# Optimization experiments

Measured on AMD Instinct MI355X. Metric: run time of the kernel, lower is better.

## Reference

```python
import jax, jax.numpy as jnp
import numpy as np

B, C, L = 4, 256, 4096
C8 = C // 8

def setup_inputs() -> dict:
    key = jax.random.key(0)
    ks = jax.random.split(key, 8)
    s = 1.0 / np.sqrt(C)
    x = jax.random.normal(ks[0], (B, C, L), dtype=jnp.float32)
    Wq = jax.random.normal(ks[1], (C8, C), dtype=jnp.float32) * s
    bq = jax.random.normal(ks[2], (C8,), dtype=jnp.float32) * s
    Wk = jax.random.normal(ks[3], (C8, C), dtype=jnp.float32) * s
    bk = jax.random.normal(ks[4], (C8,), dtype=jnp.float32) * s
    Wv = jax.random.normal(ks[5], (C, C), dtype=jnp.float32) * s
    bv = jax.random.normal(ks[6], (C,), dtype=jnp.float32) * s
    gamma = jax.random.normal(ks[7], (1,), dtype=jnp.float32) * 0.1
    return {"x": x, "Wq": Wq, "bq": bq, "Wk": Wk, "bk": bk, "Wv": Wv, "bv": bv, "gamma": gamma}

def reference(x, Wq, bq, Wk, bk, Wv, bv, gamma):
    # pointwise conv1d == channel matmul: [O,C] x [B,C,L] -> [B,O,L]
    q = jnp.einsum('oc,bcl->bol', Wq, x) + bq[None, :, None]   # [B, C8, L]
    k = jnp.einsum('oc,bcl->bol', Wk, x) + bk[None, :, None]   # [B, C8, L]
    v = jnp.einsum('oc,bcl->bol', Wv, x) + bv[None, :, None]   # [B, C,  L]
    # attention[b,i,j] = sum_c q[b,c,i] * k[b,c,j]
    attn = jnp.einsum('bci,bcj->bij', q, k)                    # [B, L, L]
    attn = jax.nn.softmax(attn, axis=-1)
    # out[b,c,i] = sum_j v[b,c,j] * attn[b,i,j]
    out = jnp.einsum('bcj,bij->bci', v, attn)                  # [B, C, L]
    return gamma * out + x
```

## Files before the change

### kernel.cpp

```cpp
#include <hip/hip_runtime.h>
#include <math.h>

#define BB 4
#define CC 256
#define LL 4096
#define DD 32
#define LOG2E 1.44269504088896f

typedef __attribute__((ext_vector_type(8))) short short8;
typedef __attribute__((ext_vector_type(4))) short short4v;
typedef __attribute__((ext_vector_type(4))) float f32x4;
typedef __attribute__((ext_vector_type(16))) float f32x16;
typedef __attribute__((ext_vector_type(4))) unsigned int uint4v;
typedef __attribute__((ext_vector_type(2))) unsigned int uint2v;

#define BARRIER() asm volatile("s_waitcnt lgkmcnt(0)\n\ts_barrier" ::: "memory")

__device__ inline float fast_exp2(float x) {
#if __has_builtin(__builtin_amdgcn_exp2f)
  return __builtin_amdgcn_exp2f(x);
#else
  return exp2f(x);
#endif
}

#define PACK8_STORE(EX0,EX1,EX2,EX3,EX4,EX5,EX6,EX7, DSTPTR)                         \
  {                                                                                  \
    unsigned pw0, pw1, pw2, pw3;                                                     \
    asm("v_cvt_pk_bf16_f32 %0, %1, %2" : "=v"(pw0) : "v"(EX0), "v"(EX1));            \
    asm("v_cvt_pk_bf16_f32 %0, %1, %2" : "=v"(pw1) : "v"(EX2), "v"(EX3));            \
    asm("v_cvt_pk_bf16_f32 %0, %1, %2" : "=v"(pw2) : "v"(EX4), "v"(EX5));            \
    asm("v_cvt_pk_bf16_f32 %0, %1, %2" : "=v"(pw3) : "v"(EX6), "v"(EX7));            \
    asm("v_permlane32_swap_b32 %0, %1" : "+v"(pw0), "+v"(pw2));                      \
    asm("v_permlane32_swap_b32 %0, %1" : "+v"(pw1), "+v"(pw3));                      \
    uint4v pu; pu.x = pw0; pu.y = pw1; pu.z = pw2; pu.w = pw3;                       \
    *(uint4v*)(DSTPTR) = pu;                                                         \
  }

__global__ __launch_bounds__(256) void wprep_kernel(
    const float* __restrict__ Wq, const float* __restrict__ Wk, const float* __restrict__ Wv,
    unsigned short* __restrict__ wf)
{
  const int t = threadIdx.x;
  const int g = blockIdx.x * 4 + (t >> 6);
  const int lane = t & 63, ql = lane & 31, hi = lane >> 5;
  const int tile = g >> 4, chunk = g & 15;
  const int cin = chunk * 16 + hi * 8;
  const float* src;
  float sc = 1.0f;
  if (tile == 0)      { src = Wq + (size_t)ql * CC; sc = LOG2E; }
  else if (tile == 1) { src = Wk + (size_t)ql * CC; }
  else                { src = Wv + (size_t)(32 * (tile - 2) + ql) * CC; }
  const f32x4 a = *(const f32x4*)(src + cin);
  const f32x4 b2 = *(const f32x4*)(src + cin + 4);
  unsigned w0, w1, w2, w3;
  const float f0 = a[0] * sc, f1 = a[1] * sc, f2 = a[2] * sc, f3 = a[3] * sc;
  const float f4 = b2[0] * sc, f5 = b2[1] * sc, f6 = b2[2] * sc, f7 = b2[3] * sc;
  asm("v_cvt_pk_bf16_f32 %0, %1, %2" : "=v"(w0) : "v"(f0), "v"(f1));
  asm("v_cvt_pk_bf16_f32 %0, %1, %2" : "=v"(w1) : "v"(f2), "v"(f3));
  asm("v_cvt_pk_bf16_f32 %0, %1, %2" : "=v"(w2) : "v"(f4), "v"(f5));
  asm("v_cvt_pk_bf16_f32 %0, %1, %2" : "=v"(w3) : "v"(f6), "v"(f7));
  uint4v u; u.x = w0; u.y = w1; u.z = w2; u.w = w3;
  *(uint4v*)(wf + ((size_t)g * 64 + lane) * 8) = u;
}

__global__ __launch_bounds__(512, 4) void qkv_kernel(
    const float* __restrict__ x, const unsigned short* __restrict__ wf,
    const float* __restrict__ bq, const float* __restrict__ bk, const float* __restrict__ bv,
    unsigned short* __restrict__ qF, unsigned short* __restrict__ kF,
    unsigned short* __restrict__ vF)
{
  __shared__ __align__(16) unsigned short xb[16 * 64 * 8];

  const int t = threadIdx.x;
  const int w = t >> 6, lane = t & 63, ql = lane & 31, hi = lane >> 5;
  const int blk = blockIdx.x;
  const int b  = (blk & 7) >> 1;
  const int it = ((blk >> 3) << 1) + (blk & 1);
  const int i0 = it * 32;

  #pragma unroll
  for (int e = 0; e < 2; ++e) {
    const int cc = 2 * w + e;
    const float* xs = x + ((size_t)(b * CC + cc * 16 + hi * 8)) * LL + i0 + ql;
    float f[8];
    #pragma unroll
    for (int j = 0; j < 8; ++j) f[j] = xs[(size_t)j * LL];
    unsigned w0, w1, w2, w3;
    asm("v_cvt_pk_bf16_f32 %0, %1, %2" : "=v"(w0) : "v"(f[0]), "v"(f[1]));
    asm("v_cvt_pk_bf16_f32 %0, %1, %2" : "=v"(w1) : "v"(f[2]), "v"(f[3]));
    asm("v_cvt_pk_bf16_f32 %0, %1, %2" : "=v"(w2) : "v"(f[4]), "v"(f[5]));
    asm("v_cvt_pk_bf16_f32 %0, %1, %2" : "=v"(w3) : "v"(f[6]), "v"(f[7]));
    uint4v u; u.x = w0; u.y = w1; u.z = w2; u.w = w3;
    *(uint4v*)&xb[(cc * 64 + lane) * 8] = u;
  }
  __syncthreads();

  const f32x16 z16 = {0.f,0.f,0.f,0.f,0.f,0.f,0.f,0.f,0.f,0.f,0.f,0.f,0.f,0.f,0.f,0.f};

  {
    f32x16 D = z16;
    #pragma unroll
    for (int c = 0; c < 16; ++c) {
      const short8 xc = *(const short8*)&xb[(c * 64 + lane) * 8];
      const short8 wv = *(const short8*)(wf + ((size_t)((2 + w) * 16 + c) * 64 + lane) * 8);
      D = __builtin_amdgcn_mfma_f32_32x32x16_bf16(xc, wv, D, 0, 0, 0);
    }
    const float bvv = bv[32 * w + ql];
    #pragma unroll
    for (int r = 0; r < 16; ++r) D[r] += bvv;
    #pragma unroll
    for (int s = 0; s < 2; ++s) {
      unsigned short* dst = vF + (((size_t)(b * 256 + 2 * it + s) * 8 + w) * 64 + lane) * 8;
      PACK8_STORE(D[8*s+0], D[8*s+1], D[8*s+2], D[8*s+3],
                  D[8*s+4], D[8*s+5], D[8*s+6], D[8*s+7], dst);
    }
  }

  if (w < 2) {
    const float* bsrc = w ? bk : bq;
    const float bscale = w ? 1.0f : LOG2E;
    float br[16];
    #pragma unroll
    for (int r = 0; r < 16; ++r)
      br[r] = bsrc[(r & 3) + 8 * (r >> 2) + 4 * hi] * bscale;
    f32x16 D = z16;
    #pragma unroll
    for (int c = 0; c < 16; ++c) {
      const short8 xc = *(const short8*)&xb[(c * 64 + lane) * 8];
      const short8 wa = *(const short8*)(wf + ((size_t)(w * 16 + c) * 64 + lane) * 8);
      D = __builtin_amdgcn_mfma_f32_32x32x16_bf16(wa, xc, D, 0, 0, 0);
    }
    #pragma unroll
    for (int r = 0; r < 16; ++r) D[r] += br[r];
    unsigned short* basef = w ? kF : qF;
    #pragma unroll
    for (int s = 0; s < 2; ++s) {
      unsigned short* dst = basef + (((size_t)(b * 128 + it) * 2 + s) * 64 + lane) * 8;
      PACK8_STORE(D[8*s+0], D[8*s+1], D[8*s+2], D[8*s+3],
                  D[8*s+4], D[8*s+5], D[8*s+6], D[8*s+7], dst);
    }
  }
}

__global__ __launch_bounds__(768, 3) void attn_kernel(
    const unsigned short* __restrict__ qF, const unsigned short* __restrict__ kF,
    const unsigned short* __restrict__ vF, const float* __restrict__ x,
    const float* __restrict__ gamma_p, float* __restrict__ out)
{
  __shared__ __align__(16) unsigned short P[2 * 8 * 2 * 2 * 512];
  __shared__ float l_lds[8][2][64];

  const int t = threadIdx.x;
  const int w = t >> 6, lane = t & 63, ql = lane & 31, hi = lane >> 5;
  const int blk = blockIdx.x;
  const int b  = (blk & 7) >> 1;
  const int it = ((blk >> 3) << 1) + (blk & 1);
  const int i0 = it * 64;

  if (w < 8) {
    const int pw = w;
    short8 qB[2][2];
    #pragma unroll
    for (int qt = 0; qt < 2; ++qt)
      #pragma unroll
      for (int c = 0; c < 2; ++c)
        qB[qt][c] = *(const short8*)(qF +
            (((size_t)(b * 128 + it * 2 + qt) * 2 + c) * 64 + lane) * 8);
    short8 kA[2];
    #pragma unroll
    for (int c = 0; c < 2; ++c)
      kA[c] = *(const short8*)(kF + (((size_t)(b * 128 + pw) * 2 + c) * 64 + lane) * 8);
    float l_r[2] = {0.f, 0.f};
    const f32x16 z16 = {0.f,0.f,0.f,0.f,0.f,0.f,0.f,0.f,0.f,0.f,0.f,0.f,0.f,0.f,0.f,0.f};

    auto produce = [&](int ss, int buf) {
      f32x16 S[2];
      __builtin_amdgcn_s_setprio(1);
      #pragma unroll
      for (int qt = 0; qt < 2; ++qt)
        S[qt] = __builtin_amdgcn_mfma_f32_32x32x16_bf16(kA[0], qB[qt][0], z16, 0, 0, 0);
      #pragma unroll
      for (int qt = 0; qt < 2; ++qt)
        S[qt] = __builtin_amdgcn_mfma_f32_32x32x16_bf16(kA[1], qB[qt][1], S[qt], 0, 0, 0);
      __builtin_amdgcn_s_setprio(0);
      const int ntile = ((ss + 1) & 15) * 8 + pw;
      #pragma unroll
      for (int c = 0; c < 2; ++c)
        kA[c] = *(const short8*)(kF + (((size_t)(b * 128 + ntile) * 2 + c) * 64 + lane) * 8);
      #pragma unroll
      for (int qt = 0; qt < 2; ++qt) {
        float ex[16];
        #pragma unroll
        for (int r = 0; r < 16; ++r) ex[r] = fast_exp2(S[qt][r]);
        l_r[qt] += ((((ex[0] + ex[1]) + (ex[2] + ex[3])) + ((ex[4] + ex[5]) + (ex[6] + ex[7])))
                 + (((ex[8] + ex[9]) + (ex[10] + ex[11])) + ((ex[12] + ex[13]) + (ex[14] + ex[15]))));
        #pragma unroll
        for (int c = 0; c < 2; ++c) {
          unsigned short* dst = &P[(((buf * 8 + pw) * 2 + qt) * 2 + c) * 512 + hi * 256 + ql * 8];
          PACK8_STORE(ex[8*c+0], ex[8*c+1], ex[8*c+2], ex[8*c+3],
                      ex[8*c+4], ex[8*c+5], ex[8*c+6], ex[8*c+7], dst);
        }
      }
    };

    produce(0, 0);
    __syncthreads();
    for (int i = 0; i < 16; ++i) {
      if (i < 15) produce(i + 1, (i + 1) & 1);
      BARRIER();
    }
    l_lds[pw][0][lane] = l_r[0];
    l_lds[pw][1][lane] = l_r[1];
    BARRIER();
  } else {
    const int mq = w - 8;
    const unsigned short* vroot = vF + (size_t)b * (256 * 8 * 512) + lane * 8;
    f32x16 O[2][2];
    #pragma unroll
    for (int mi = 0; mi < 2; ++mi)
      #pragma unroll
      for (int qt = 0; qt < 2; ++qt) {
        const f32x16 z16 = {0.f,0.f,0.f,0.f,0.f,0.f,0.f,0.f,0.f,0.f,0.f,0.f,0.f,0.f,0.f,0.f};
        O[mi][qt] = z16;
      }
    short8 vA[8][2];
    #pragma unroll
    for (int s = 0; s < 8; ++s)
      #pragma unroll
      for (int mi = 0; mi < 2; ++mi)
        vA[s][mi] = *(const short8*)(vroot + ((size_t)(s * 8 + 2 * mq + mi)) * 512);
    __syncthreads();

    short8 pb[3][2];
    for (int i = 0; i < 16; ++i) {
      const int buf = i & 1;
      #pragma unroll
      for (int s = 0; s < 2; ++s)
        #pragma unroll
        for (int qt = 0; qt < 2; ++qt)
          pb[s][qt] = *(const short8*)(&P[((((buf * 8 + 0) * 2 + qt) * 2 + s) * 512)
                                          + hi * 256 + ql * 8]);
      #pragma unroll
      for (int s = 0; s < 16; ++s) {
        if (s < 14) {
          const int ns = s + 2, kk = ns >> 1, c = ns & 1;
          #pragma unroll
          for (int qt = 0; qt < 2; ++qt)
            pb[ns % 3][qt] = *(const short8*)(&P[((((buf * 8 + kk) * 2 + qt) * 2 + c) * 512)
                                                 + hi * 256 + ql * 8]);
        }
        __builtin_amdgcn_s_setprio(1);
        #pragma unroll
        for (int mi = 0; mi < 2; ++mi)
          #pragma unroll
          for (int qt = 0; qt < 2; ++qt)
            O[mi][qt] = __builtin_amdgcn_mfma_f32_32x32x16_bf16(vA[s & 7][mi], pb[s % 3][qt],
                                                                O[mi][qt], 0, 0, 0);
        __builtin_amdgcn_s_setprio(0);
        const int kg = (i * 16 + s + 8) & 255;
        #pragma unroll
        for (int mi = 0; mi < 2; ++mi)
          vA[s & 7][mi] = *(const short8*)(vroot + ((size_t)(kg * 8 + 2 * mq + mi)) * 512);
      }
      BARRIER();
    }
    BARRIER();

    const float gam = gamma_p[0];
    float inv_l[2];
    #pragma unroll
    for (int qt = 0; qt < 2; ++qt) {
      float s = 0.f;
      #pragma unroll
      for (int pw = 0; pw < 8; ++pw)
        s += l_lds[pw][qt][ql] + l_lds[pw][qt][ql + 32];
      inv_l[qt] = 1.0f / s;
    }
    #pragma unroll
    for (int mi = 0; mi < 2; ++mi)
      #pragma unroll
      for (int qt = 0; qt < 2; ++qt)
        #pragma unroll
        for (int r = 0; r < 16; ++r) {
          const int ch = 64 * mq + 32 * mi + (r & 3) + 8 * (r >> 2) + 4 * hi;
          const int ii = i0 + 32 * qt + ql;
          const size_t idx = ((size_t)b * CC + ch) * LL + ii;
          out[idx] = gam * O[mi][qt][r] * inv_l[qt] + x[idx];
        }
  }
}

extern "C" void kernel_launch(void* const* d_in, const int* in_sizes, int n_in,
                              void* d_out, int out_size, void* d_ws, size_t ws_size,
                              hipStream_t stream) {
  const float* x     = (const float*)d_in[0];
  const float* Wq    = (const float*)d_in[1];
  const float* bq    = (const float*)d_in[2];
  const float* Wk    = (const float*)d_in[3];
  const float* bk    = (const float*)d_in[4];
  const float* Wv    = (const float*)d_in[5];
  const float* bv    = (const float*)d_in[6];
  const float* gamma = (const float*)d_in[7];
  float* out = (float*)d_out;

  unsigned short* qF = (unsigned short*)d_ws;
  unsigned short* kF = qF + (size_t)BB * LL * DD;
  unsigned short* vF = kF + (size_t)BB * LL * DD;
  unsigned short* wf = (unsigned short*)d_out;

  wprep_kernel<<<40, 256, 0, stream>>>(Wq, Wk, Wv, wf);
  qkv_kernel<<<512, 512, 0, stream>>>(x, wf, bq, bk, bv, qF, kF, vF);
  attn_kernel<<<256, 768, 0, stream>>>(qF, kF, vF, x, gamma, out);
}
```

Measured before the change: 129.6 us.

## Fuse QKV projection and attention into one cooperative kernel with grid sync

Merges the separate QKV projection kernel and the attention kernel into one kernel launched cooperatively with 256 blocks of 768 threads. Each block first computes Q, K and V for its 64 positions, with LDS shared between phases through a union. A grid-wide sync then precedes the attention phase. This removes one kernel launch and the gap between kernels, at the cost of a grid barrier and cooperative-launch overhead, and it requires every block to be resident at once.

```diff
diff --git a/kernel.cpp b/kernel.cpp
--- a/kernel.cpp
+++ b/kernel.cpp
@@ -1,5 +1,8 @@
 #include <hip/hip_runtime.h>
+#include <hip/hip_cooperative_groups.h>
 #include <math.h>
+
+namespace cg = cooperative_groups;
 
 #define BB 4
 #define CC 256
@@ -8,11 +11,9 @@
 #define LOG2E 1.44269504088896f
 
 typedef __attribute__((ext_vector_type(8))) short short8;
-typedef __attribute__((ext_vector_type(4))) short short4v;
 typedef __attribute__((ext_vector_type(4))) float f32x4;
 typedef __attribute__((ext_vector_type(16))) float f32x16;
 typedef __attribute__((ext_vector_type(4))) unsigned int uint4v;
-typedef __attribute__((ext_vector_type(2))) unsigned int uint2v;
 
 #define BARRIER() asm volatile("s_waitcnt lgkmcnt(0)\n\ts_barrier" ::: "memory")
 
@@ -53,9 +54,9 @@
   else                { src = Wv + (size_t)(32 * (tile - 2) + ql) * CC; }
   const f32x4 a = *(const f32x4*)(src + cin);
   const f32x4 b2 = *(const f32x4*)(src + cin + 4);
-  unsigned w0, w1, w2, w3;
   const float f0 = a[0] * sc, f1 = a[1] * sc, f2 = a[2] * sc, f3 = a[3] * sc;
   const float f4 = b2[0] * sc, f5 = b2[1] * sc, f6 = b2[2] * sc, f7 = b2[3] * sc;
+  unsigned w0, w1, w2, w3;
   asm("v_cvt_pk_bf16_f32 %0, %1, %2" : "=v"(w0) : "v"(f0), "v"(f1));
   asm("v_cvt_pk_bf16_f32 %0, %1, %2" : "=v"(w1) : "v"(f2), "v"(f3));
   asm("v_cvt_pk_bf16_f32 %0, %1, %2" : "=v"(w2) : "v"(f4), "v"(f5));
@@ -64,92 +65,20 @@
   *(uint4v*)(wf + ((size_t)g * 64 + lane) * 8) = u;
 }
 
-__global__ __launch_bounds__(512, 4) void qkv_kernel(
+__global__ __launch_bounds__(768, 3) void fused_kernel(
     const float* __restrict__ x, const unsigned short* __restrict__ wf,
     const float* __restrict__ bq, const float* __restrict__ bk, const float* __restrict__ bv,
     unsigned short* __restrict__ qF, unsigned short* __restrict__ kF,
-    unsigned short* __restrict__ vF)
+    unsigned short* __restrict__ vF, const float* __restrict__ gamma_p,
+    float* __restrict__ out)
 {
-  __shared__ __align__(16) unsigned short xb[16 * 64 * 8];
-
-  const int t = threadIdx.x;
-  const int w = t >> 6, lane = t & 63, ql = lane & 31, hi = lane >> 5;
-  const int blk = blockIdx.x;
-  const int b  = (blk & 7) >> 1;
-  const int it = ((blk >> 3) << 1) + (blk & 1);
-  const int i0 = it * 32;
-
-  #pragma unroll
-  for (int e = 0; e < 2; ++e) {
-    const int cc = 2 * w + e;
-    const float* xs = x + ((size_t)(b * CC + cc * 16 + hi * 8)) * LL + i0 + ql;
-    float f[8];
-    #pragma unroll
-    for (int j = 0; j < 8; ++j) f[j] = xs[(size_t)j * LL];
-    unsigned w0, w1, w2, w3;
-    asm("v_cvt_pk_bf16_f32 %0, %1, %2" : "=v"(w0) : "v"(f[0]), "v"(f[1]));
-    asm("v_cvt_pk_bf16_f32 %0, %1, %2" : "=v"(w1) : "v"(f[2]), "v"(f[3]));
-    asm("v_cvt_pk_bf16_f32 %0, %1, %2" : "=v"(w2) : "v"(f[4]), "v"(f[5]));
-    asm("v_cvt_pk_bf16_f32 %0, %1, %2" : "=v"(w3) : "v"(f[6]), "v"(f[7]));
-    uint4v u; u.x = w0; u.y = w1; u.z = w2; u.w = w3;
-    *(uint4v*)&xb[(cc * 64 + lane) * 8] = u;
-  }
-  __syncthreads();
-
-  const f32x16 z16 = {0.f,0.f,0.f,0.f,0.f,0.f,0.f,0.f,0.f,0.f,0.f,0.f,0.f,0.f,0.f,0.f};
-
-  {
-    f32x16 D = z16;
-    #pragma unroll
-    for (int c = 0; c < 16; ++c) {
-      const short8 xc = *(const short8*)&xb[(c * 64 + lane) * 8];
-      const short8 wv = *(const short8*)(wf + ((size_t)((2 + w) * 16 + c) * 64 + lane) * 8);
-      D = __builtin_amdgcn_mfma_f32_32x32x16_bf16(xc, wv, D, 0, 0, 0);
-    }
-    const float bvv = bv[32 * w + ql];
-    #pragma unroll
-    for (int r = 0; r < 16; ++r) D[r] += bvv;
-    #pragma unroll
-    for (int s = 0; s < 2; ++s) {
-      unsigned short* dst = vF + (((size_t)(b * 256 + 2 * it + s) * 8 + w) * 64 + lane) * 8;
-      PACK8_STORE(D[8*s+0], D[8*s+1], D[8*s+2], D[8*s+3],
-                  D[8*s+4], D[8*s+5], D[8*s+6], D[8*s+7], dst);
-    }
-  }
-
-  if (w < 2) {
-    const float* bsrc = w ? bk : bq;
-    const float bscale = w ? 1.0f : LOG2E;
-    float br[16];
-    #pragma unroll
-    for (int r = 0; r < 16; ++r)
-      br[r] = bsrc[(r & 3) + 8 * (r >> 2) + 4 * hi] * bscale;
-    f32x16 D = z16;
-    #pragma unroll
-    for (int c = 0; c < 16; ++c) {
-      const short8 xc = *(const short8*)&xb[(c * 64 + lane) * 8];
-      const short8 wa = *(const short8*)(wf + ((size_t)(w * 16 + c) * 64 + lane) * 8);
-      D = __builtin_amdgcn_mfma_f32_32x32x16_bf16(wa, xc, D, 0, 0, 0);
-    }
-    #pragma unroll
-    for (int r = 0; r < 16; ++r) D[r] += br[r];
-    unsigned short* basef = w ? kF : qF;
-    #pragma unroll
-    for (int s = 0; s < 2; ++s) {
-      unsigned short* dst = basef + (((size_t)(b * 128 + it) * 2 + s) * 64 + lane) * 8;
-      PACK8_STORE(D[8*s+0], D[8*s+1], D[8*s+2], D[8*s+3],
-                  D[8*s+4], D[8*s+5], D[8*s+6], D[8*s+7], dst);
-    }
-  }
-}
-
-__global__ __launch_bounds__(768, 3) void attn_kernel(
-    const unsigned short* __restrict__ qF, const unsigned short* __restrict__ kF,
-    const unsigned short* __restrict__ vF, const float* __restrict__ x,
-    const float* __restrict__ gamma_p, float* __restrict__ out)
-{
-  __shared__ __align__(16) unsigned short P[2 * 8 * 2 * 2 * 512];
-  __shared__ float l_lds[8][2][64];
+  __shared__ union __align__(16) {
+    unsigned short xb[2 * 16 * 64 * 8];
+    struct {
+      unsigned short P[2 * 8 * 2 * 2 * 512];
+      float l[8][2][64];
+    } a;
+  } sm;
 
   const int t = threadIdx.x;
   const int w = t >> 6, lane = t & 63, ql = lane & 31, hi = lane >> 5;
@@ -157,6 +86,80 @@
   const int b  = (blk & 7) >> 1;
   const int it = ((blk >> 3) << 1) + (blk & 1);
   const int i0 = it * 64;
+  const f32x16 z16 = {0.f,0.f,0.f,0.f,0.f,0.f,0.f,0.f,0.f,0.f,0.f,0.f,0.f,0.f,0.f,0.f};
+
+  {
+    const int nst = (w < 8) ? 2 : 4;
+    const int sub = (w < 8) ? 0 : 1;
+    const int c0  = (w < 8) ? 2 * w : 4 * (w - 8);
+    #pragma unroll 4
+    for (int e = 0; e < nst; ++e) {
+      const int cc = c0 + e;
+      const float* xs = x + ((size_t)(b * CC + cc * 16 + hi * 8)) * LL + i0 + sub * 32 + ql;
+      float f[8];
+      #pragma unroll
+      for (int j = 0; j < 8; ++j) f[j] = xs[(size_t)j * LL];
+      unsigned w0, w1, w2, w3;
+      asm("v_cvt_pk_bf16_f32 %0, %1, %2" : "=v"(w0) : "v"(f[0]), "v"(f[1]));
+      asm("v_cvt_pk_bf16_f32 %0, %1, %2" : "=v"(w1) : "v"(f[2]), "v"(f[3]));
+      asm("v_cvt_pk_bf16_f32 %0, %1, %2" : "=v"(w2) : "v"(f[4]), "v"(f[5]));
+      asm("v_cvt_pk_bf16_f32 %0, %1, %2" : "=v"(w3) : "v"(f[6]), "v"(f[7]));
+      uint4v u; u.x = w0; u.y = w1; u.z = w2; u.w = w3;
+      *(uint4v*)&sm.xb[((sub * 16 + cc) * 64 + lane) * 8] = u;
+    }
+  }
+  __syncthreads();
+
+  if (w < 8) {
+    const float bvv = bv[32 * w + ql];
+    #pragma unroll
+    for (int sub = 0; sub < 2; ++sub) {
+      f32x16 D = z16;
+      #pragma unroll
+      for (int c = 0; c < 16; ++c) {
+        const short8 xc = *(const short8*)&sm.xb[((sub * 16 + c) * 64 + lane) * 8];
+        const short8 wv = *(const short8*)(wf + ((size_t)((2 + w) * 16 + c) * 64 + lane) * 8);
+        D = __builtin_amdgcn_mfma_f32_32x32x16_bf16(xc, wv, D, 0, 0, 0);
+      }
+      #pragma unroll
+      for (int r = 0; r < 16; ++r) D[r] += bvv;
+      #pragma unroll
+      for (int s2 = 0; s2 < 2; ++s2) {
+        unsigned short* dst =
+            vF + (((size_t)(b * 256 + 4 * it + 2 * sub + s2) * 8 + w) * 64 + lane) * 8;
+        PACK8_STORE(D[8*s2+0], D[8*s2+1], D[8*s2+2], D[8*s2+3],
+                    D[8*s2+4], D[8*s2+5], D[8*s2+6], D[8*s2+7], dst);
+      }
+    }
+  } else {
+    const int wq = w - 8, sub = wq >> 1, which = wq & 1;
+    const float* bsrc = which ? bk : bq;
+    const float bscale = which ? 1.0f : LOG2E;
+    float br[16];
+    #pragma unroll
+    for (int r = 0; r < 16; ++r)
+      br[r] = bsrc[(r & 3) + 8 * (r >> 2) + 4 * hi] * bscale;
+    f32x16 D = z16;
+    #pragma unroll
+    for (int c = 0; c < 16; ++c) {
+      const short8 xc = *(const short8*)&sm.xb[((sub * 16 + c) * 64 + lane) * 8];
+      const short8 wa = *(const short8*)(wf + ((size_t)(which * 16 + c) * 64 + lane) * 8);
+      D = __builtin_amdgcn_mfma_f32_32x32x16_bf16(wa, xc, D, 0, 0, 0);
+    }
+    #pragma unroll
+    for (int r = 0; r < 16; ++r) D[r] += br[r];
+    unsigned short* basef = which ? kF : qF;
+    const int tile32 = 2 * it + sub;
+    #pragma unroll
+    for (int s2 = 0; s2 < 2; ++s2) {
+      unsigned short* dst = basef + (((size_t)(b * 128 + tile32) * 2 + s2) * 64 + lane) * 8;
+      PACK8_STORE(D[8*s2+0], D[8*s2+1], D[8*s2+2], D[8*s2+3],
+                  D[8*s2+4], D[8*s2+5], D[8*s2+6], D[8*s2+7], dst);
+    }
+  }
+
+  __threadfence();
+  cg::this_grid().sync();
 
   if (w < 8) {
     const int pw = w;
@@ -172,7 +175,6 @@
     for (int c = 0; c < 2; ++c)
       kA[c] = *(const short8*)(kF + (((size_t)(b * 128 + pw) * 2 + c) * 64 + lane) * 8);
     float l_r[2] = {0.f, 0.f};
-    const f32x16 z16 = {0.f,0.f,0.f,0.f,0.f,0.f,0.f,0.f,0.f,0.f,0.f,0.f,0.f,0.f,0.f,0.f};
 
     auto produce = [&](int ss, int buf) {
       f32x16 S[2];
@@ -197,7 +199,8 @@
                  + (((ex[8] + ex[9]) + (ex[10] + ex[11])) + ((ex[12] + ex[13]) + (ex[14] + ex[15]))));
         #pragma unroll
         for (int c = 0; c < 2; ++c) {
-          unsigned short* dst = &P[(((buf * 8 + pw) * 2 + qt) * 2 + c) * 512 + hi * 256 + ql * 8];
+          unsigned short* dst =
+              &sm.a.P[(((buf * 8 + pw) * 2 + qt) * 2 + c) * 512 + hi * 256 + ql * 8];
           PACK8_STORE(ex[8*c+0], ex[8*c+1], ex[8*c+2], ex[8*c+3],
                       ex[8*c+4], ex[8*c+5], ex[8*c+6], ex[8*c+7], dst);
         }
@@ -210,8 +213,8 @@
       if (i < 15) produce(i + 1, (i + 1) & 1);
       BARRIER();
     }
-    l_lds[pw][0][lane] = l_r[0];
-    l_lds[pw][1][lane] = l_r[1];
+    sm.a.l[pw][0][lane] = l_r[0];
+    sm.a.l[pw][1][lane] = l_r[1];
     BARRIER();
   } else {
     const int mq = w - 8;
@@ -220,10 +223,7 @@
     #pragma unroll
     for (int mi = 0; mi < 2; ++mi)
       #pragma unroll
-      for (int qt = 0; qt < 2; ++qt) {
-        const f32x16 z16 = {0.f,0.f,0.f,0.f,0.f,0.f,0.f,0.f,0.f,0.f,0.f,0.f,0.f,0.f,0.f,0.f};
-        O[mi][qt] = z16;
-      }
+      for (int qt = 0; qt < 2; ++qt) O[mi][qt] = z16;
     short8 vA[8][2];
     #pragma unroll
     for (int s = 0; s < 8; ++s)
@@ -239,16 +239,16 @@
       for (int s = 0; s < 2; ++s)
         #pragma unroll
         for (int qt = 0; qt < 2; ++qt)
-          pb[s][qt] = *(const short8*)(&P[((((buf * 8 + 0) * 2 + qt) * 2 + s) * 512)
-                                          + hi * 256 + ql * 8]);
+          pb[s][qt] = *(const short8*)(&sm.a.P[((((buf * 8 + 0) * 2 + qt) * 2 + s) * 512)
+                                               + hi * 256 + ql * 8]);
       #pragma unroll
       for (int s = 0; s < 16; ++s) {
         if (s < 14) {
           const int ns = s + 2, kk = ns >> 1, c = ns & 1;
           #pragma unroll
           for (int qt = 0; qt < 2; ++qt)
-            pb[ns % 3][qt] = *(const short8*)(&P[((((buf * 8 + kk) * 2 + qt) * 2 + c) * 512)
-                                                 + hi * 256 + ql * 8]);
+            pb[ns % 3][qt] = *(const short8*)(&sm.a.P[((((buf * 8 + kk) * 2 + qt) * 2 + c) * 512)
+                                                      + hi * 256 + ql * 8]);
         }
         __builtin_amdgcn_s_setprio(1);
         #pragma unroll
@@ -274,7 +274,7 @@
       float s = 0.f;
       #pragma unroll
       for (int pw = 0; pw < 8; ++pw)
-        s += l_lds[pw][qt][ql] + l_lds[pw][qt][ql + 32];
+        s += sm.a.l[pw][qt][ql] + sm.a.l[pw][qt][ql + 32];
       inv_l[qt] = 1.0f / s;
     }
     #pragma unroll
@@ -308,8 +308,12 @@
   unsigned short* kF = qF + (size_t)BB * LL * DD;
   unsigned short* vF = kF + (size_t)BB * LL * DD;
   unsigned short* wf = (unsigned short*)d_out;
+  const unsigned short* wf_c = wf;
 
   wprep_kernel<<<40, 256, 0, stream>>>(Wq, Wk, Wv, wf);
-  qkv_kernel<<<512, 512, 0, stream>>>(x, wf, bq, bk, bv, qF, kF, vF);
-  attn_kernel<<<256, 768, 0, stream>>>(qF, kF, vF, x, gamma, out);
+
+  void* args[] = {(void*)&x, (void*)&wf_c, (void*)&bq, (void*)&bk, (void*)&bv,
+                  (void*)&qF, (void*)&kF, (void*)&vF, (void*)&gamma, (void*)&out};
+  hipLaunchCooperativeKernel((const void*)fused_kernel, dim3(256), dim3(768),
+                             args, 0, stream);
 }
```

New measurement: 264.1 us. 2.04x slower.
